# Optimization experiments

Hardware: AMD Instinct MI355X
Metric: run time of the kernel (lower is better)

## Reference

```python
import jax, jax.numpy as jnp
import numpy as np

B, S, HID = 2, 2048, 768
H, DH = 12, 64
WINDOW = 128
THETA = 10000.0
NEG_INF = -1e9  # keras MHA uses -1e9 additive mask


def _rope(x, theta=THETA):
    """Apply rotary embedding. x: [B, S, H, DH] (rotate over last dim)."""
    s, d = x.shape[1], x.shape[-1]
    inv_freq = 1.0 / (theta ** (jnp.arange(0, d, 2, dtype=jnp.float32) / d))  # [d/2]
    ang = jnp.arange(s, dtype=jnp.float32)[:, None] * inv_freq[None, :]       # [S, d/2]
    cos = jnp.concatenate([jnp.cos(ang), jnp.cos(ang)], axis=-1)[None, :, None, :]  # [1,S,1,d]
    sin = jnp.concatenate([jnp.sin(ang), jnp.sin(ang)], axis=-1)[None, :, None, :]
    x1, x2 = x[..., : d // 2], x[..., d // 2 :]
    rot = jnp.concatenate([-x2, x1], axis=-1)
    return x * cos + rot * sin


def setup_inputs() -> dict:
    key = jax.random.key(0)
    ks = jax.random.split(key, 9)
    std = 0.02
    hidden_states = jax.random.normal(ks[0], (B, S, HID), dtype=jnp.float32)
    attention_mask = jnp.ones((B, S), dtype=jnp.int32)
    Wq = std * jax.random.truncated_normal(ks[1], -2.0, 2.0, (HID, H, DH), dtype=jnp.float32)
    Wk = std * jax.random.truncated_normal(ks[2], -2.0, 2.0, (HID, H, DH), dtype=jnp.float32)
    Wv = std * jax.random.truncated_normal(ks[3], -2.0, 2.0, (HID, H, DH), dtype=jnp.float32)
    Wo = std * jax.random.truncated_normal(ks[4], -2.0, 2.0, (H, DH, HID), dtype=jnp.float32)
    bq = jnp.zeros((H, DH), dtype=jnp.float32)
    bk = jnp.zeros((H, DH), dtype=jnp.float32)
    bv = jnp.zeros((H, DH), dtype=jnp.float32)
    bo = jnp.zeros((HID,), dtype=jnp.float32)
    return {"hidden_states": hidden_states, "attention_mask": attention_mask,
            "Wq": Wq, "bq": bq, "Wk": Wk, "bk": bk, "Wv": Wv, "bv": bv, "Wo": Wo, "bo": bo}


def reference(hidden_states, attention_mask, Wq, bq, Wk, bk, Wv, bv, Wo, bo):
    b, s, _ = hidden_states.shape
    # RoPE applied to raw hidden states split into heads (as in source), then flattened back
    x4 = hidden_states.reshape(b, s, H, DH)
    q_in = _rope(x4).reshape(b, s, HID)
    k_in = _rope(x4).reshape(b, s, HID)
    v_in = hidden_states
    # keras MultiHeadAttention projections
    q = jnp.einsum("bsi,ihd->bshd", q_in, Wq) + bq
    k = jnp.einsum("bsi,ihd->bshd", k_in, Wk) + bk
    v = jnp.einsum("bsi,ihd->bshd", v_in, Wv) + bv
    q = q * (1.0 / jnp.sqrt(jnp.float32(DH)))
    scores = jnp.einsum("bqhd,bkhd->bhqk", q, k)  # [B,H,S,S]
    # combined mask: padding [B,1,1,S] AND sliding window [S,S]
    pad = attention_mask.astype(bool)[:, None, None, :]
    pos = jnp.arange(s, dtype=jnp.int32)
    win = (jnp.abs(pos[:, None] - pos[None, :]) < WINDOW)[None, None, :, :]
    mask = jnp.logical_and(pad, win)
    scores = scores + (1.0 - mask.astype(scores.dtype)) * NEG_INF
    attn = jax.nn.softmax(scores, axis=-1)
    out = jnp.einsum("bhqk,bkhd->bqhd", attn, v)
    return jnp.einsum("bqhd,hdi->bqi", out, Wo) + bo
```

## Files before the change

kernel.cpp:

```cpp
#include <hip/hip_runtime.h>
#include <hip/hip_bf16.h>
#include <math.h>

#define NB 2
#define NS 2048
#define NHID 768
#define NH 12
#define NDH 64
#define NWIN 128

typedef __attribute__((ext_vector_type(8))) short bf16x8;
typedef __attribute__((ext_vector_type(4))) float f32x4;

__device__ inline unsigned short f2b(float f) {
    union { float f; unsigned int i; } x; x.f = f;
    unsigned int r = x.i + 0x7FFFu + ((x.i >> 16) & 1u);
    return (unsigned short)(r >> 16);
}
__device__ inline int xcd_remap(int flat, int nwg) {
    return (flat & 7) * (nwg >> 3) + (flat >> 3);
}
__device__ __forceinline__ void gload_lds16(const void* g, void* l) {
    __builtin_amdgcn_global_load_lds((const __attribute__((address_space(1))) void*)g,
                                     (__attribute__((address_space(3))) void*)l, 16, 0, 0);
}

__global__ __launch_bounds__(256) void k_prep(const float* __restrict__ x,
                                              __hip_bfloat16* __restrict__ rb,
                                              __hip_bfloat16* __restrict__ xb,
                                              const float* __restrict__ w0, const float* __restrict__ w1,
                                              const float* __restrict__ w2, const float* __restrict__ w3,
                                              __hip_bfloat16* o0, __hip_bfloat16* o1,
                                              __hip_bfloat16* o2, __hip_bfloat16* o3) {
    int bid = blockIdx.x;
    int t = threadIdx.x;
    if (bid < 576) {
        int wsel = bid / 144, r = bid % 144;
        int kx = r % 12, ny = r / 12;
        const float* W; __hip_bfloat16* O;
        switch (wsel) {
            case 0: W = w0; O = o0; break;
            case 1: W = w1; O = o1; break;
            case 2: W = w2; O = o2; break;
            default: W = w3; O = o3; break;
        }
        __shared__ float tile[64][65];
        int k0 = kx * 64, n0 = ny * 64;
        int rr = t >> 4, cc = (t & 15) * 4;
#pragma unroll
        for (int u = 0; u < 4; ++u) {
            int row = rr + u * 16;
            float4 f = *(const float4*)(W + (size_t)(k0 + row) * NHID + n0 + cc);
            tile[row][cc] = f.x; tile[row][cc + 1] = f.y;
            tile[row][cc + 2] = f.z; tile[row][cc + 3] = f.w;
        }
        __syncthreads();
#pragma unroll
        for (int u = 0; u < 4; ++u) {
            int n = rr + u * 16;
            ushort4 s = { f2b(tile[cc + 0][n]), f2b(tile[cc + 1][n]),
                          f2b(tile[cc + 2][n]), f2b(tile[cc + 3][n]) };
            *(ushort4*)((unsigned short*)O + (size_t)(n0 + n) * NHID + k0 + cc) = s;
        }
    } else {
        int idx = (bid - 576) * 256 + t;
        int f = idx & 31;
        int h = (idx >> 5) % NH;
        int bs = idx / (32 * NH);
        int s = bs & (NS - 1);
        int base = bs * NHID + h * NDH;
        float x1 = x[base + f], x2 = x[base + 32 + f];
        float inv = exp2f(-0.4152410118609203f * (float)f);
        float ang = (float)s * inv;
        float c = cosf(ang), sn = sinf(ang);
        ((unsigned short*)rb)[base + f]      = f2b(x1 * c - x2 * sn);
        ((unsigned short*)rb)[base + 32 + f] = f2b(x2 * c + x1 * sn);
        ((unsigned short*)xb)[base + f]      = f2b(x1);
        ((unsigned short*)xb)[base + 32 + f] = f2b(x2);
    }
}

union Frag { bf16x8 v; unsigned long long q[2]; uint4 u; };

template<int MF>
__device__ __forceinline__ void gemm_body(const __hip_bfloat16* __restrict__ A,
                                          const __hip_bfloat16* __restrict__ Wt,
                                          const float* __restrict__ bias,
                                          __hip_bfloat16* __restrict__ Cb,
                                          float* __restrict__ Cf, float scale,
                                          int m0, int n0) {
    constexpr int BM = 32 * MF;
    __shared__ __attribute__((aligned(16))) unsigned short As[BM][64];
    __shared__ __attribute__((aligned(16))) unsigned short Bs[64][64];
    const int t = threadIdx.x;
    const int wid = t >> 6, lane = t & 63;
    const int wm = (wid >> 1) * 16 * MF, wn = (wid & 1) * 32;
    const int g = lane >> 4, r16 = lane & 15;
    const int swz = r16 & 7;

    f32x4 acc[MF][2];
#pragma unroll
    for (int i = 0; i < MF; ++i)
#pragma unroll
        for (int j = 0; j < 2; ++j) acc[i][j] = (f32x4){0.f, 0.f, 0.f, 0.f};

    const int srow = t >> 3;
    const int gslot = (t & 7) ^ (srow & 7);
    const unsigned short* gA = (const unsigned short*)A + (size_t)(m0 + srow) * NHID + gslot * 8;
    const unsigned short* gB = (const unsigned short*)Wt + (size_t)(n0 + srow) * NHID + gslot * 8;
    char* lA = (char*)&As[0][0] + wid * 1024;
    char* lB = (char*)&Bs[0][0] + wid * 1024;

    for (int ks = 0; ks < NHID / 64; ++ks) {
        __syncthreads();
#pragma unroll
        for (int c = 0; c < MF; ++c)
            gload_lds16(gA + (size_t)c * 32 * NHID + ks * 64, lA + c * 4096);
#pragma unroll
        for (int c = 0; c < 2; ++c)
            gload_lds16(gB + (size_t)c * 32 * NHID + ks * 64, lB + c * 4096);
        __syncthreads();
#pragma unroll
        for (int kk = 0; kk < 2; ++kk) {
            Frag af[MF], bf[2];
#pragma unroll
            for (int mi = 0; mi < MF; ++mi)
                af[mi].u = *(const uint4*)&As[wm + mi * 16 + r16][((kk * 4 + g) ^ swz) * 8];
#pragma unroll
            for (int ni = 0; ni < 2; ++ni)
                bf[ni].u = *(const uint4*)&Bs[wn + ni * 16 + r16][((kk * 4 + g) ^ swz) * 8];
#pragma unroll
            for (int mi = 0; mi < MF; ++mi)
#pragma unroll
                for (int ni = 0; ni < 2; ++ni)
                    acc[mi][ni] = __builtin_amdgcn_mfma_f32_16x16x32_bf16(af[mi].v, bf[ni].v, acc[mi][ni], 0, 0, 0);
        }
    }

#pragma unroll
    for (int mi = 0; mi < MF; ++mi)
#pragma unroll
        for (int ni = 0; ni < 2; ++ni)
#pragma unroll
            for (int r = 0; r < 4; ++r) {
                int m = m0 + wm + mi * 16 + 4 * g + r;
                int n = n0 + wn + ni * 16 + r16;
                float v = (acc[mi][ni][r] + bias[n]) * scale;
                if (Cb) ((unsigned short*)Cb)[(size_t)m * NHID + n] = f2b(v);
                else    Cf[(size_t)m * NHID + n] = v;
            }
}

__global__ __launch_bounds__(256) void k_gemm_qkv(const __hip_bfloat16* __restrict__ rb,
                                                  const __hip_bfloat16* __restrict__ xb,
                                                  const __hip_bfloat16* __restrict__ WtQ,
                                                  const __hip_bfloat16* __restrict__ WtK,
                                                  const __hip_bfloat16* __restrict__ WtV,
                                                  const float* __restrict__ bq,
                                                  const float* __restrict__ bk,
                                                  const float* __restrict__ bv,
                                                  __hip_bfloat16* qb, __hip_bfloat16* kb,
                                                  __hip_bfloat16* vb) {
    int flat = blockIdx.x + 12 * blockIdx.y + 384 * blockIdx.z;
    int id = xcd_remap(flat, 1152);
    int z = id / 384, rem = id - z * 384;
    int ty = rem / 12, tx = rem - ty * 12;
    const __hip_bfloat16 *A, *W; const float* bias; __hip_bfloat16* C; float scale;
    switch (z) {
        case 0:  A = rb; W = WtQ; bias = bq; C = qb; scale = 0.125f; break;
        case 1:  A = rb; W = WtK; bias = bk; C = kb; scale = 1.0f;   break;
        default: A = xb; W = WtV; bias = bv; C = vb; scale = 1.0f;   break;
    }
    gemm_body<4>(A, W, bias, C, nullptr, scale, ty * 128, tx * 64);
}

__global__ __launch_bounds__(256) void k_gemm_out(const __hip_bfloat16* __restrict__ A,
                                                  const __hip_bfloat16* __restrict__ Wt,
                                                  const float* __restrict__ bias,
                                                  float* __restrict__ Cf) {
    int flat = blockIdx.x + 12 * blockIdx.y;
    int id = xcd_remap(flat, 768);
    int ty = id / 12, tx = id - ty * 12;
    gemm_body<2>(A, Wt, bias, nullptr, Cf, 1.0f, ty * 64, tx * 64);
}

__global__ __launch_bounds__(256) void k_attn(const __hip_bfloat16* __restrict__ q,
                                              const __hip_bfloat16* __restrict__ kmat,
                                              const __hip_bfloat16* __restrict__ vmat,
                                              const int* __restrict__ am,
                                              __hip_bfloat16* __restrict__ o) {
    __shared__ unsigned short Ks[64][72];
    __shared__ unsigned short Vt[64][72];
    __shared__ float kmask[64];
    const int t = threadIdx.x;
    const int h = blockIdx.y, b = blockIdx.z;
    const int i0 = blockIdx.x * 64;
    const int w = t >> 6, lane = t & 63;
    const int g = lane >> 4, r16 = lane & 15;
    const int qrow = i0 + w * 16 + r16;

    Frag qf[2];
    {
        const unsigned short* qp = (const unsigned short*)q + ((size_t)(b * NS) + qrow) * NHID + h * NDH;
        qf[0].q[0] = *(const unsigned long long*)(qp + 4 * g);
        qf[0].q[1] = *(const unsigned long long*)(qp + 16 + 4 * g);
        qf[1].q[0] = *(const unsigned long long*)(qp + 32 + 4 * g);
        qf[1].q[1] = *(const unsigned long long*)(qp + 48 + 4 * g);
    }
    float m_run = -1e30f, l_run = 0.f;
    f32x4 oacc[4];
#pragma unroll
    for (int i = 0; i < 4; ++i) oacc[i] = (f32x4){0.f, 0.f, 0.f, 0.f};

    const int ktL = (i0 == 0) ? 2 : (i0 == 64) ? 1 : 0;
    const int ktH = (i0 == NS - 64) ? 2 : (i0 == NS - 128) ? 3 : 4;

    uint4 pK0, pK1, pV0, pV1; float pm = 0.f;

#define LOADREGS(KT) do {                                                        \
    int j0_ = i0 - 128 + (KT) * 64;                                              \
    const unsigned short* kp_ = (const unsigned short*)kmat +                    \
        ((size_t)(b * NS) + j0_ + (t >> 2)) * NHID + h * NDH + (t & 3) * 16;     \
    pK0 = *(const uint4*)kp_;                                                    \
    pK1 = *(const uint4*)(kp_ + 8);                                              \
    const unsigned short* vp_ = (const unsigned short*)vmat +                    \
        ((size_t)(b * NS) + j0_ + 2 * (t & 31)) * NHID + h * NDH + (t >> 5) * 8; \
    pV0 = *(const uint4*)vp_;                                                    \
    pV1 = *(const uint4*)(vp_ + NHID);                                           \
    if (t < 64) pm = (am[b * NS + j0_ + t] != 0) ? 0.f : -1e30f;                 \
} while (0)

    LOADREGS(ktL);
    for (int kt = ktL; kt <= ktH; ++kt) {
        const int j0 = i0 - 128 + kt * 64;
        {
            *(uint4*)&Ks[t >> 2][(t & 3) * 16]     = pK0;
            *(uint4*)&Ks[t >> 2][(t & 3) * 16 + 8] = pK1;
            union { uint4 u; unsigned short s[8]; } a0, a1;
            a0.u = pV0; a1.u = pV1;
#pragma unroll
            for (int e = 0; e < 8; ++e) {
                unsigned int pk = (unsigned int)a0.s[e] | ((unsigned int)a1.s[e] << 16);
                *(unsigned int*)&Vt[(t >> 5) * 8 + e][2 * (t & 31)] = pk;
            }
            if (t < 64) kmask[t] = pm;
        }
        if (kt < ktH) LOADREGS(kt + 1);
        asm volatile("s_waitcnt lgkmcnt(0)" ::: "memory");
        __builtin_amdgcn_s_barrier();

        f32x4 sacc[4];
#pragma unroll
        for (int i = 0; i < 4; ++i) sacc[i] = (f32x4){0.f, 0.f, 0.f, 0.f};
#pragma unroll
        for (int mi = 0; mi < 4; ++mi) {
            Frag kf0, kf1;
            const unsigned short* pk = &Ks[mi * 16 + r16][0];
            kf0.q[0] = *(const unsigned long long*)(pk + 4 * g);
            kf0.q[1] = *(const unsigned long long*)(pk + 16 + 4 * g);
            kf1.q[0] = *(const unsigned long long*)(pk + 32 + 4 * g);
            kf1.q[1] = *(const unsigned long long*)(pk + 48 + 4 * g);
            sacc[mi] = __builtin_amdgcn_mfma_f32_16x16x32_bf16(kf0.v, qf[0].v, sacc[mi], 0, 0, 0);
            sacc[mi] = __builtin_amdgcn_mfma_f32_16x16x32_bf16(kf1.v, qf[1].v, sacc[mi], 0, 0, 0);
        }

        float p[4][4];
        float tmax = -1e30f;
#pragma unroll
        for (int mi = 0; mi < 4; ++mi)
#pragma unroll
            for (int r = 0; r < 4; ++r) {
                int key = j0 + mi * 16 + 4 * g + r;
                float s = sacc[mi][r] + kmask[mi * 16 + 4 * g + r];
                int d = qrow - key; d = d < 0 ? -d : d;
                if (d >= NWIN) s = -1e30f;
                p[mi][r] = s;
                tmax = fmaxf(tmax, s);
            }
        tmax = fmaxf(tmax, __shfl_xor(tmax, 16));
        tmax = fmaxf(tmax, __shfl_xor(tmax, 32));
        float mnew = fmaxf(m_run, tmax);
        float psum = 0.f;
#pragma unroll
        for (int mi = 0; mi < 4; ++mi)
#pragma unroll
            for (int r = 0; r < 4; ++r) {
                float pv = __expf(p[mi][r] - mnew);
                p[mi][r] = pv;
                psum += pv;
            }
        psum += __shfl_xor(psum, 16);
        psum += __shfl_xor(psum, 32);
        float alpha = __expf(m_run - mnew);
        m_run = mnew;
        l_run = l_run * alpha + psum;
#pragma unroll
        for (int mi = 0; mi < 4; ++mi)
#pragma unroll
            for (int r = 0; r < 4; ++r) oacc[mi][r] *= alpha;

        Frag pf[2];
#pragma unroll
        for (int ks2 = 0; ks2 < 2; ++ks2) {
            union { bf16x8 v; unsigned short s[8]; } pp;
#pragma unroll
            for (int r = 0; r < 4; ++r) {
                pp.s[r]     = f2b(p[2 * ks2][r]);
                pp.s[r + 4] = f2b(p[2 * ks2 + 1][r]);
            }
            pf[ks2].v = pp.v;
        }

#pragma unroll
        for (int mi = 0; mi < 4; ++mi) {
            Frag vf0, vf1;
            const unsigned short* pv = &Vt[mi * 16 + r16][0];
            vf0.q[0] = *(const unsigned long long*)(pv + 4 * g);
            vf0.q[1] = *(const unsigned long long*)(pv + 16 + 4 * g);
            vf1.q[0] = *(const unsigned long long*)(pv + 32 + 4 * g);
            vf1.q[1] = *(const unsigned long long*)(pv + 48 + 4 * g);
            oacc[mi] = __builtin_amdgcn_mfma_f32_16x16x32_bf16(vf0.v, pf[0].v, oacc[mi], 0, 0, 0);
            oacc[mi] = __builtin_amdgcn_mfma_f32_16x16x32_bf16(vf1.v, pf[1].v, oacc[mi], 0, 0, 0);
        }
        asm volatile("s_waitcnt lgkmcnt(0)" ::: "memory");
        __builtin_amdgcn_s_barrier();
    }
#undef LOADREGS

    float inv_l = 1.0f / l_run;
    unsigned short* op = (unsigned short*)o + ((size_t)(b * NS) + qrow) * NHID + h * NDH;
#pragma unroll
    for (int mi = 0; mi < 4; ++mi) {
        ushort4 s = { f2b(oacc[mi][0] * inv_l), f2b(oacc[mi][1] * inv_l),
                      f2b(oacc[mi][2] * inv_l), f2b(oacc[mi][3] * inv_l) };
        *(ushort4*)(op + mi * 16 + 4 * g) = s;
    }
}

extern "C" void kernel_launch(void* const* d_in, const int* in_sizes, int n_in,
                              void* d_out, int out_size, void* d_ws, size_t ws_size,
                              hipStream_t stream) {
    (void)in_sizes; (void)n_in; (void)out_size; (void)ws_size;
    const float* x  = (const float*)d_in[0];
    const int*   am = (const int*)d_in[1];
    const float* Wq = (const float*)d_in[2];
    const float* bq = (const float*)d_in[3];
    const float* Wk = (const float*)d_in[4];
    const float* bk = (const float*)d_in[5];
    const float* Wv = (const float*)d_in[6];
    const float* bv = (const float*)d_in[7];
    const float* Wo = (const float*)d_in[8];
    const float* bo = (const float*)d_in[9];
    float* out = (float*)d_out;
    float* ws  = (float*)d_ws;

    __hip_bfloat16* rb  = (__hip_bfloat16*)(ws);
    __hip_bfloat16* xb  = (__hip_bfloat16*)(ws + 1572864);
    __hip_bfloat16* WtQ = (__hip_bfloat16*)(ws + 3145728);
    __hip_bfloat16* WtK = (__hip_bfloat16*)(ws + 3440640);
    __hip_bfloat16* WtV = (__hip_bfloat16*)(ws + 3735552);
    __hip_bfloat16* WtO = (__hip_bfloat16*)(ws + 4030464);
    __hip_bfloat16* qb  = (__hip_bfloat16*)(ws + 4325376);
    __hip_bfloat16* kb  = (__hip_bfloat16*)(ws + 5898240);
    __hip_bfloat16* vb  = (__hip_bfloat16*)(ws + 7471104);
    __hip_bfloat16* aob = (__hip_bfloat16*)(ws + 9043968);

    k_prep<<<576 + 6144, 256, 0, stream>>>(x, rb, xb, Wq, Wk, Wv, Wo, WtQ, WtK, WtV, WtO);
    dim3 gq(NHID / 64, NB * NS / 128, 3);
    k_gemm_qkv<<<gq, 256, 0, stream>>>(rb, xb, WtQ, WtK, WtV, bq, bk, bv, qb, kb, vb);
    dim3 ga(NS / 64, NH, NB);
    k_attn<<<ga, 256, 0, stream>>>(qb, kb, vb, am, aob);
    dim3 gg(NHID / 64, NB * NS / 64);
    k_gemm_out<<<gg, 256, 0, stream>>>(aob, WtO, bo, out);
}
```

Baseline: 64.51 us.

## Rewrite projection GEMMs as single-wave 64x64 tiles with double-buffered LDS

The QKV and output-projection GEMMs now use one 64-thread wavefront per block. Each block computes a 64x64 tile with a 4x4 MFMA accumulator grid and loads 32-wide K slices into two LDS buffers. Loads for the next slice are issued before computing the current one, with explicit vmcnt waits in place of workgroup barriers, to overlap memory with MFMA and drop __syncthreads. The cost is more, smaller blocks, higher register pressure per wave, and reliance on manual vmcnt counting for correctness.

```diff
diff --git a/kernel.cpp b/kernel.cpp
--- a/kernel.cpp
+++ b/kernel.cpp
@@ -24,6 +24,8 @@
     __builtin_amdgcn_global_load_lds((const __attribute__((address_space(1))) void*)g,
                                      (__attribute__((address_space(3))) void*)l, 16, 0, 0);
 }
+
+union Frag { bf16x8 v; unsigned long long q[2]; uint4 u; };
 
 __global__ __launch_bounds__(256) void k_prep(const float* __restrict__ x,
                                               __hip_bfloat16* __restrict__ rb,
@@ -80,108 +82,113 @@
     }
 }
 
-union Frag { bf16x8 v; unsigned long long q[2]; uint4 u; };
-
-template<int MF>
-__device__ __forceinline__ void gemm_body(const __hip_bfloat16* __restrict__ A,
-                                          const __hip_bfloat16* __restrict__ Wt,
-                                          const float* __restrict__ bias,
-                                          __hip_bfloat16* __restrict__ Cb,
-                                          float* __restrict__ Cf, float scale,
-                                          int m0, int n0) {
-    constexpr int BM = 32 * MF;
-    __shared__ __attribute__((aligned(16))) unsigned short As[BM][64];
-    __shared__ __attribute__((aligned(16))) unsigned short Bs[64][64];
+__device__ __forceinline__ void gemm1w(const __hip_bfloat16* __restrict__ A,
+                                       const __hip_bfloat16* __restrict__ Wt,
+                                       const float* __restrict__ bias,
+                                       __hip_bfloat16* __restrict__ Cb,
+                                       float* __restrict__ Cf, float scale,
+                                       int m0, int n0) {
+    __shared__ __attribute__((aligned(16))) unsigned short As[2][64][32];
+    __shared__ __attribute__((aligned(16))) unsigned short Bs[2][64][32];
     const int t = threadIdx.x;
-    const int wid = t >> 6, lane = t & 63;
-    const int wm = (wid >> 1) * 16 * MF, wn = (wid & 1) * 32;
-    const int g = lane >> 4, r16 = lane & 15;
-    const int swz = r16 & 7;
-
-    f32x4 acc[MF][2];
-#pragma unroll
-    for (int i = 0; i < MF; ++i)
-#pragma unroll
-        for (int j = 0; j < 2; ++j) acc[i][j] = (f32x4){0.f, 0.f, 0.f, 0.f};
-
-    const int srow = t >> 3;
-    const int gslot = (t & 7) ^ (srow & 7);
+    const int g = t >> 4, r16 = t & 15;
+    const int rho = (r16 >> 1) & 3;
+
+    f32x4 acc[4][4];
+#pragma unroll
+    for (int i = 0; i < 4; ++i)
+#pragma unroll
+        for (int j = 0; j < 4; ++j) acc[i][j] = (f32x4){0.f, 0.f, 0.f, 0.f};
+
+    const int srow = t >> 2;
+    const int gslot = (t & 3) ^ ((t >> 3) & 3);
     const unsigned short* gA = (const unsigned short*)A + (size_t)(m0 + srow) * NHID + gslot * 8;
     const unsigned short* gB = (const unsigned short*)Wt + (size_t)(n0 + srow) * NHID + gslot * 8;
-    char* lA = (char*)&As[0][0] + wid * 1024;
-    char* lB = (char*)&Bs[0][0] + wid * 1024;
-
-    for (int ks = 0; ks < NHID / 64; ++ks) {
-        __syncthreads();
-#pragma unroll
-        for (int c = 0; c < MF; ++c)
-            gload_lds16(gA + (size_t)c * 32 * NHID + ks * 64, lA + c * 4096);
-#pragma unroll
-        for (int c = 0; c < 2; ++c)
-            gload_lds16(gB + (size_t)c * 32 * NHID + ks * 64, lB + c * 4096);
-        __syncthreads();
-#pragma unroll
-        for (int kk = 0; kk < 2; ++kk) {
-            Frag af[MF], bf[2];
-#pragma unroll
-            for (int mi = 0; mi < MF; ++mi)
-                af[mi].u = *(const uint4*)&As[wm + mi * 16 + r16][((kk * 4 + g) ^ swz) * 8];
-#pragma unroll
-            for (int ni = 0; ni < 2; ++ni)
-                bf[ni].u = *(const uint4*)&Bs[wn + ni * 16 + r16][((kk * 4 + g) ^ swz) * 8];
-#pragma unroll
-            for (int mi = 0; mi < MF; ++mi)
-#pragma unroll
-                for (int ni = 0; ni < 2; ++ni)
-                    acc[mi][ni] = __builtin_amdgcn_mfma_f32_16x16x32_bf16(af[mi].v, bf[ni].v, acc[mi][ni], 0, 0, 0);
-        }
-    }
-
-#pragma unroll
-    for (int mi = 0; mi < MF; ++mi)
-#pragma unroll
-        for (int ni = 0; ni < 2; ++ni)
+
+#define STAGE1(b, tt) do {                                                      \
+    _Pragma("unroll")                                                           \
+    for (int c = 0; c < 4; ++c)                                                 \
+        gload_lds16(gA + (size_t)c * 16 * NHID + (tt) * 32, (char*)&As[b][0][0] + c * 1024); \
+    _Pragma("unroll")                                                           \
+    for (int c = 0; c < 4; ++c)                                                 \
+        gload_lds16(gB + (size_t)c * 16 * NHID + (tt) * 32, (char*)&Bs[b][0][0] + c * 1024); \
+} while (0)
+
+#define COMPUTE1(b) do {                                                        \
+    Frag af[4], bf[4];                                                          \
+    _Pragma("unroll")                                                           \
+    for (int mi = 0; mi < 4; ++mi)                                              \
+        af[mi].u = *(const uint4*)&As[b][mi * 16 + r16][(g ^ rho) * 8];         \
+    _Pragma("unroll")                                                           \
+    for (int ni = 0; ni < 4; ++ni)                                              \
+        bf[ni].u = *(const uint4*)&Bs[b][ni * 16 + r16][(g ^ rho) * 8];         \
+    _Pragma("unroll")                                                           \
+    for (int mi = 0; mi < 4; ++mi)                                              \
+        _Pragma("unroll")                                                       \
+        for (int ni = 0; ni < 4; ++ni)                                          \
+            acc[mi][ni] = __builtin_amdgcn_mfma_f32_16x16x32_bf16(af[mi].v, bf[ni].v, acc[mi][ni], 0, 0, 0); \
+} while (0)
+
+    STAGE1(0, 0);
+#pragma unroll
+    for (int it = 0; it < 12; ++it) {
+        STAGE1(1, 2 * it + 1);
+        asm volatile("s_waitcnt vmcnt(8)" ::: "memory");
+        COMPUTE1(0);
+        if (it < 11) {
+            STAGE1(0, 2 * it + 2);
+            asm volatile("s_waitcnt vmcnt(8)" ::: "memory");
+        } else {
+            asm volatile("s_waitcnt vmcnt(0)" ::: "memory");
+        }
+        COMPUTE1(1);
+    }
+#undef STAGE1
+#undef COMPUTE1
+
+#pragma unroll
+    for (int mi = 0; mi < 4; ++mi)
+#pragma unroll
+        for (int ni = 0; ni < 4; ++ni)
 #pragma unroll
             for (int r = 0; r < 4; ++r) {
-                int m = m0 + wm + mi * 16 + 4 * g + r;
-                int n = n0 + wn + ni * 16 + r16;
+                int m = m0 + mi * 16 + 4 * g + r;
+                int n = n0 + ni * 16 + r16;
                 float v = (acc[mi][ni][r] + bias[n]) * scale;
                 if (Cb) ((unsigned short*)Cb)[(size_t)m * NHID + n] = f2b(v);
                 else    Cf[(size_t)m * NHID + n] = v;
             }
 }
 
-__global__ __launch_bounds__(256) void k_gemm_qkv(const __hip_bfloat16* __restrict__ rb,
-                                                  const __hip_bfloat16* __restrict__ xb,
-                                                  const __hip_bfloat16* __restrict__ WtQ,
-                                                  const __hip_bfloat16* __restrict__ WtK,
-                                                  const __hip_bfloat16* __restrict__ WtV,
-                                                  const float* __restrict__ bq,
-                                                  const float* __restrict__ bk,
-                                                  const float* __restrict__ bv,
-                                                  __hip_bfloat16* qb, __hip_bfloat16* kb,
-                                                  __hip_bfloat16* vb) {
-    int flat = blockIdx.x + 12 * blockIdx.y + 384 * blockIdx.z;
-    int id = xcd_remap(flat, 1152);
-    int z = id / 384, rem = id - z * 384;
-    int ty = rem / 12, tx = rem - ty * 12;
+__global__ __launch_bounds__(64) void k_gemm_qkv(const __hip_bfloat16* __restrict__ rb,
+                                                 const __hip_bfloat16* __restrict__ xb,
+                                                 const __hip_bfloat16* __restrict__ WtQ,
+                                                 const __hip_bfloat16* __restrict__ WtK,
+                                                 const __hip_bfloat16* __restrict__ WtV,
+                                                 const float* __restrict__ bq,
+                                                 const float* __restrict__ bk,
+                                                 const float* __restrict__ bv,
+                                                 __hip_bfloat16* qb, __hip_bfloat16* kb,
+                                                 __hip_bfloat16* vb) {
+    int id = xcd_remap(blockIdx.x, 2304);
+    int z = id / 768, rem = id % 768;
+    int ty = rem / 12, tx = rem % 12;
     const __hip_bfloat16 *A, *W; const float* bias; __hip_bfloat16* C; float scale;
     switch (z) {
         case 0:  A = rb; W = WtQ; bias = bq; C = qb; scale = 0.125f; break;
         case 1:  A = rb; W = WtK; bias = bk; C = kb; scale = 1.0f;   break;
         default: A = xb; W = WtV; bias = bv; C = vb; scale = 1.0f;   break;
     }
-    gemm_body<4>(A, W, bias, C, nullptr, scale, ty * 128, tx * 64);
-}
-
-__global__ __launch_bounds__(256) void k_gemm_out(const __hip_bfloat16* __restrict__ A,
-                                                  const __hip_bfloat16* __restrict__ Wt,
-                                                  const float* __restrict__ bias,
-                                                  float* __restrict__ Cf) {
-    int flat = blockIdx.x + 12 * blockIdx.y;
-    int id = xcd_remap(flat, 768);
-    int ty = id / 12, tx = id - ty * 12;
-    gemm_body<2>(A, Wt, bias, nullptr, Cf, 1.0f, ty * 64, tx * 64);
+    gemm1w(A, W, bias, C, nullptr, scale, ty * 64, tx * 64);
+}
+
+__global__ __launch_bounds__(64) void k_gemm_out(const __hip_bfloat16* __restrict__ A,
+                                                 const __hip_bfloat16* __restrict__ Wt,
+                                                 const float* __restrict__ bias,
+                                                 float* __restrict__ Cf) {
+    int id = xcd_remap(blockIdx.x, 768);
+    int ty = id / 12, tx = id % 12;
+    gemm1w(A, Wt, bias, nullptr, Cf, 1.0f, ty * 64, tx * 64);
 }
 
 __global__ __launch_bounds__(256) void k_attn(const __hip_bfloat16* __restrict__ q,
@@ -366,10 +373,8 @@
     __hip_bfloat16* aob = (__hip_bfloat16*)(ws + 9043968);
 
     k_prep<<<576 + 6144, 256, 0, stream>>>(x, rb, xb, Wq, Wk, Wv, Wo, WtQ, WtK, WtV, WtO);
-    dim3 gq(NHID / 64, NB * NS / 128, 3);
-    k_gemm_qkv<<<gq, 256, 0, stream>>>(rb, xb, WtQ, WtK, WtV, bq, bk, bv, qb, kb, vb);
+    k_gemm_qkv<<<2304, 64, 0, stream>>>(rb, xb, WtQ, WtK, WtV, bq, bk, bv, qb, kb, vb);
     dim3 ga(NS / 64, NH, NB);
     k_attn<<<ga, 256, 0, stream>>>(qb, kb, vb, am, aob);
-    dim3 gg(NHID / 64, NB * NS / 64);
-    k_gemm_out<<<gg, 256, 0, stream>>>(aob, WtO, bo, out);
-}
+    k_gemm_out<<<768, 64, 0, stream>>>(aob, WtO, bo, out);
+}
```

Result: slower. 84.39 us (+30.8%).
